# Optimization experiments

Measured on AMD Instinct MI355X. Metric: run time of the kernel, lower is better.

## Reference

```python
import jax, jax.numpy as jnp
import numpy as np

NUM_EXPERTS = 8
HIDDEN = 1024
TOKENS = 8192


def setup_inputs() -> dict:
    key = jax.random.key(0)
    k1, k2, k3, k4 = jax.random.split(key, 4)
    inp = jax.random.normal(k1, (TOKENS, HIDDEN), dtype=jnp.float32)
    gate = jax.random.normal(k2, (TOKENS, NUM_EXPERTS), dtype=jnp.float32)
    # expert parameters: one dense layer per expert (H -> H)
    W = jax.random.normal(k3, (NUM_EXPERTS, HIDDEN, HIDDEN), dtype=jnp.float32) / np.sqrt(HIDDEN)
    b = jax.random.normal(k4, (NUM_EXPERTS, HIDDEN), dtype=jnp.float32) * 0.01
    return {"input": inp, "gate": gate, "W": W, "b": b}


def reference(input, gate, W, b):
    # Routing: softmax over router logits, top-1 expert per token.
    probs = jax.nn.softmax(gate, axis=-1)            # [T, E]
    expert_idx = jnp.argmax(probs, axis=-1)          # [T]
    top_p = jnp.take_along_axis(probs, expert_idx[:, None], axis=-1)[:, 0]  # [T]

    # Dispatch + grouped GEMM (computed densely for all experts, then masked):
    # y[e, t, d] = input[t, :] @ W[e] + b[e]
    y = jnp.einsum("th,ehd->etd", input, W) + b[:, None, :]  # [E, T, H]

    # Combine: select the routed expert's output, scaled by its gate prob.
    dispatch = jax.nn.one_hot(expert_idx, NUM_EXPERTS, dtype=input.dtype) * top_p[:, None]  # [T, E]
    out = jnp.einsum("etd,te->td", y, dispatch)      # [T, H]
    return out
```

## Files before the change

kernel.cpp:

```cpp
#include <hip/hip_runtime.h>
#include <hip/hip_bf16.h>
#include <cstdint>
#include <cstddef>

#define TOK 8192
#define HID 1024
#define NE 8

typedef __bf16 bf16x4 __attribute__((ext_vector_type(4)));
typedef __bf16 bf16x8 __attribute__((ext_vector_type(8)));
typedef float floatx4 __attribute__((ext_vector_type(4)));

static __device__ __forceinline__ __bf16 f2bf(float x) {
    unsigned u = __builtin_bit_cast(unsigned, x);
    u += 0x7fffu + ((u >> 16) & 1u);
    unsigned short hs = (unsigned short)(u >> 16);
    return __builtin_bit_cast(__bf16, hs);
}

__global__ void prep_kernel(const float* __restrict__ X, const float* __restrict__ gate,
                            const float* __restrict__ W,
                            __bf16* __restrict__ Xb, __bf16* __restrict__ Wt,
                            float* __restrict__ scale, int* __restrict__ counts,
                            int* __restrict__ list) {
    const int b = blockIdx.x;
    const int t = threadIdx.x;

    if (b < 4096) {
        size_t idx = (size_t)b * 256 + t;
        const float4 a0 = *(const float4*)(X + idx * 8);
        const float4 a1 = *(const float4*)(X + idx * 8 + 4);
        bf16x8 v;
        v[0] = f2bf(a0.x); v[1] = f2bf(a0.y); v[2] = f2bf(a0.z); v[3] = f2bf(a0.w);
        v[4] = f2bf(a1.x); v[5] = f2bf(a1.y); v[6] = f2bf(a1.z); v[7] = f2bf(a1.w);
        *(bf16x8*)(Xb + idx * 8) = v;

        if (b < 32) {
            __shared__ int hcnt[NE];
            __shared__ int hbase[NE];
            if (t < NE) hcnt[t] = 0;
            __syncthreads();
            int tok = b * 256 + t;
            float g[NE];
#pragma unroll
            for (int j = 0; j < NE; j++) g[j] = gate[tok * NE + j];
            float gm = g[0]; int best = 0;
#pragma unroll
            for (int j = 1; j < NE; j++) {
                if (g[j] > gm) { gm = g[j]; best = j; }
            }
            float s = 0.f;
#pragma unroll
            for (int j = 0; j < NE; j++) s += __expf(g[j] - gm);
            scale[tok] = 1.0f / s;
            int lpos = atomicAdd(&hcnt[best], 1);
            __syncthreads();
            if (t < NE) hbase[t] = atomicAdd(&counts[t], hcnt[t]);
            __syncthreads();
            list[best * TOK + hbase[best] + lpos] = tok;
        }
    } else {
        const int bb = b - 4096;
        const int e = bb >> 8;
        const int tk = (bb >> 4) & 15;
        const int tn = bb & 15;
        const int k0 = tk * 64, n0 = tn * 64;

        __shared__ float ld[64][65];
        {
            const int r4 = t >> 4, c4 = t & 15;
#pragma unroll
            for (int i = 0; i < 4; i++) {
                int kl = r4 + 16 * i;
                float4 v = *(const float4*)(W + ((size_t)e * HID + (k0 + kl)) * HID + n0 + c4 * 4);
                ld[kl][c4 * 4 + 0] = v.x; ld[kl][c4 * 4 + 1] = v.y;
                ld[kl][c4 * 4 + 2] = v.z; ld[kl][c4 * 4 + 3] = v.w;
            }
        }
        __syncthreads();
        {
            const int nl = t >> 2, kc2 = t & 3;
#pragma unroll
            for (int h = 0; h < 2; h++) {
                int c = kc2 + 4 * h;
                bf16x8 v;
#pragma unroll
                for (int j = 0; j < 8; j++) v[j] = f2bf(ld[c * 8 + j][nl]);
                *(bf16x8*)(Wt + ((size_t)e * HID + n0 + nl) * HID + k0 + c * 8) = v;
            }
        }
    }
}

__launch_bounds__(256)
__global__ void moe_gemm_bf16(const __bf16* __restrict__ Xb, const __bf16* __restrict__ Wt,
                              const float* __restrict__ Bias, const float* __restrict__ scale,
                              const int* __restrict__ counts, const int* __restrict__ list,
                              float* __restrict__ out) {
    const int bid = blockIdx.x;
    const int nt = bid & 7;
    const int mt = (bid >> 3) & 63;
    const int e  = bid >> 9;

    const int cnt = counts[e];
    if (mt * 128 >= cnt) return;
    const int mvalid = min(128, cnt - mt * 128);
    const int n0 = nt * 128;

    __shared__ __bf16 As[128 * 64];
    __shared__ __bf16 Bs[128 * 64];
    __shared__ int   tok[128];
    __shared__ float scl[128];

    const int tid  = threadIdx.x;
    const int lane = tid & 63;
    const int wave = tid >> 6;

    if (tid < 128) {
        int g = mt * 128 + tid;
        int tk = (g < cnt) ? list[e * TOK + g] : 0;
        tok[tid] = tk;
        scl[tid] = (g < cnt) ? scale[tk] : 0.f;
    }
    __syncthreads();

    const int srow = lane >> 3;
    const int gchunk = ((lane & 7) ^ srow) * 8;
    const __bf16* aptr[4];
    const __bf16* bptr[4];
#pragma unroll
    for (int i = 0; i < 4; i++) {
        int r = wave * 32 + i * 8 + srow;
        aptr[i] = Xb + (size_t)tok[r] * HID + gchunk;
        bptr[i] = Wt + ((size_t)e * HID + n0 + r) * HID + gchunk;
    }

    const int ln = lane & 15;
    const int q  = lane >> 4;
    const int wm = (wave >> 1) * 64;
    const int wn = (wave & 1) * 64;
    const int rsw = ln & 7;

    floatx4 acc[4][4];
#pragma unroll
    for (int mi = 0; mi < 4; mi++)
#pragma unroll
        for (int ni = 0; ni < 4; ni++) acc[mi][ni] = (floatx4){0.f, 0.f, 0.f, 0.f};

    for (int k0 = 0; k0 < HID; k0 += 64) {
#pragma unroll
        for (int i = 0; i < 4; i++) {
            __builtin_amdgcn_global_load_lds(
                (const __attribute__((address_space(1))) void*)(aptr[i] + k0),
                (__attribute__((address_space(3))) void*)(&As[(wave * 32 + i * 8) * 64]),
                16, 0, 0);
            __builtin_amdgcn_global_load_lds(
                (const __attribute__((address_space(1))) void*)(bptr[i] + k0),
                (__attribute__((address_space(3))) void*)(&Bs[(wave * 32 + i * 8) * 64]),
                16, 0, 0);
        }
        __syncthreads();

#pragma unroll
        for (int kk = 0; kk < 64; kk += 32) {
            const int cb = (kk >> 3) + q;
            const int pos = (cb ^ rsw) * 8;
            bf16x8 af[4], bfv[4];
#pragma unroll
            for (int mi = 0; mi < 4; mi++)
                af[mi] = *(const bf16x8*)(&As[(wm + mi * 16 + ln) * 64 + pos]);
#pragma unroll
            for (int ni = 0; ni < 4; ni++)
                bfv[ni] = *(const bf16x8*)(&Bs[(wn + ni * 16 + ln) * 64 + pos]);
#pragma unroll
            for (int mi = 0; mi < 4; mi++)
#pragma unroll
                for (int ni = 0; ni < 4; ni++)
                    acc[mi][ni] = __builtin_amdgcn_mfma_f32_16x16x32_bf16(
                        af[mi], bfv[ni], acc[mi][ni], 0, 0, 0);
        }
        __syncthreads();
    }

    float bn[4];
#pragma unroll
    for (int ni = 0; ni < 4; ni++) bn[ni] = Bias[e * HID + n0 + wn + ni * 16 + ln];

#pragma unroll
    for (int mi = 0; mi < 4; mi++) {
#pragma unroll
        for (int r = 0; r < 4; r++) {
            int row = wm + mi * 16 + q * 4 + r;
            if (row < mvalid) {
                int t = tok[row];
                float sc = scl[row];
                size_t ob = (size_t)t * HID + n0 + wn + ln;
#pragma unroll
                for (int ni = 0; ni < 4; ni++)
                    out[ob + ni * 16] = sc * (acc[mi][ni][r] + bn[ni]);
            }
        }
    }
}

__launch_bounds__(256)
__global__ void moe_gemm_fb(const float* __restrict__ X, const float* __restrict__ W,
                            const float* __restrict__ Bias, const float* __restrict__ scale,
                            const int* __restrict__ counts, const int* __restrict__ list,
                            float* __restrict__ out) {
    const int bid = blockIdx.x;
    const int e  = bid >> 9;
    const int nt = (bid >> 6) & 7;
    const int mt = bid & 63;
    const int cnt = counts[e];
    if (mt * 128 >= cnt) return;
    const int mvalid = min(128, cnt - mt * 128);
    const int n0 = nt * 128;

    __shared__ __bf16 As[128 * 64];
    __shared__ __bf16 Bs[128 * 64];
    __shared__ int   tok[128];
    __shared__ float scl[128];

    const int tid = threadIdx.x;
    if (tid < 128) {
        int g = mt * 128 + tid;
        int tk = (g < cnt) ? list[e * TOK + g] : 0;
        tok[tid] = tk;
        scl[tid] = (g < cnt) ? scale[tk] : 0.f;
    }
    __syncthreads();

    const int c4 = tid & 15;
    const float* rp[8];
    bool rv[8];
#pragma unroll
    for (int i = 0; i < 8; i++) {
        int m = (tid >> 4) + 16 * i;
        rv[i] = (m < mvalid);
        rp[i] = X + (size_t)tok[m] * HID;
    }
    const int n4 = tid & 31;
    const int kb = tid >> 5;
    const float* wbase = W + (size_t)e * HID * HID + (size_t)(kb * 8) * HID + n0 + n4 * 4;

    const int lane = tid & 63;
    const int ln = lane & 15;
    const int q  = lane >> 4;
    const int wave = tid >> 6;
    const int wm = (wave >> 1) * 64;
    const int wn = (wave & 1) * 64;

    floatx4 acc[4][4];
#pragma unroll
    for (int mi = 0; mi < 4; mi++)
#pragma unroll
        for (int ni = 0; ni < 4; ni++) acc[mi][ni] = (floatx4){0.f, 0.f, 0.f, 0.f};

    for (int k0 = 0; k0 < HID; k0 += 64) {
#pragma unroll
        for (int i = 0; i < 8; i++) {
            int m = (tid >> 4) + 16 * i;
            float4 v = make_float4(0.f, 0.f, 0.f, 0.f);
            if (rv[i]) v = *(const float4*)(rp[i] + k0 + c4 * 4);
            bf16x4 b4;
            b4[0] = f2bf(v.x); b4[1] = f2bf(v.y); b4[2] = f2bf(v.z); b4[3] = f2bf(v.w);
            int chunk = c4 >> 1;
            int addr = m * 64 + ((chunk ^ (m & 7)) * 8) + (c4 & 1) * 4;
            *(bf16x4*)(&As[addr]) = b4;
        }
        {
            const float* wp = wbase + (size_t)k0 * HID;
            float4 rr[8];
#pragma unroll
            for (int r = 0; r < 8; r++) rr[r] = *(const float4*)(wp + (size_t)r * HID);
#pragma unroll
            for (int j = 0; j < 4; j++) {
                int n = n4 * 4 + j;
                int c = kb ^ (n & 7);
                bf16x8 pk;
                pk[0] = f2bf(j == 0 ? rr[0].x : j == 1 ? rr[0].y : j == 2 ? rr[0].z : rr[0].w);
                pk[1] = f2bf(j == 0 ? rr[1].x : j == 1 ? rr[1].y : j == 2 ? rr[1].z : rr[1].w);
                pk[2] = f2bf(j == 0 ? rr[2].x : j == 1 ? rr[2].y : j == 2 ? rr[2].z : rr[2].w);
                pk[3] = f2bf(j == 0 ? rr[3].x : j == 1 ? rr[3].y : j == 2 ? rr[3].z : rr[3].w);
                pk[4] = f2bf(j == 0 ? rr[4].x : j == 1 ? rr[4].y : j == 2 ? rr[4].z : rr[4].w);
                pk[5] = f2bf(j == 0 ? rr[5].x : j == 1 ? rr[5].y : j == 2 ? rr[5].z : rr[5].w);
                pk[6] = f2bf(j == 0 ? rr[6].x : j == 1 ? rr[6].y : j == 2 ? rr[6].z : rr[6].w);
                pk[7] = f2bf(j == 0 ? rr[7].x : j == 1 ? rr[7].y : j == 2 ? rr[7].z : rr[7].w);
                *(bf16x8*)(&Bs[n * 64 + c * 8]) = pk;
            }
        }
        __syncthreads();
#pragma unroll
        for (int kk = 0; kk < 64; kk += 32) {
            const int cbase = (kk >> 3) + q;
            bf16x8 af[4], bfv[4];
#pragma unroll
            for (int mi = 0; mi < 4; mi++) {
                int row = wm + mi * 16 + ln;
                af[mi] = *(const bf16x8*)(&As[row * 64 + ((cbase ^ (row & 7)) * 8)]);
            }
#pragma unroll
            for (int ni = 0; ni < 4; ni++) {
                int n = wn + ni * 16 + ln;
                bfv[ni] = *(const bf16x8*)(&Bs[n * 64 + ((cbase ^ (n & 7)) * 8)]);
            }
#pragma unroll
            for (int mi = 0; mi < 4; mi++)
#pragma unroll
                for (int ni = 0; ni < 4; ni++)
                    acc[mi][ni] = __builtin_amdgcn_mfma_f32_16x16x32_bf16(
                        af[mi], bfv[ni], acc[mi][ni], 0, 0, 0);
        }
        __syncthreads();
    }

    float bn[4];
#pragma unroll
    for (int ni = 0; ni < 4; ni++) bn[ni] = Bias[e * HID + n0 + wn + ni * 16 + ln];
#pragma unroll
    for (int mi = 0; mi < 4; mi++) {
#pragma unroll
        for (int r = 0; r < 4; r++) {
            int row = wm + mi * 16 + q * 4 + r;
            if (row < mvalid) {
                int t = tok[row];
                float sc = scl[row];
                size_t ob = (size_t)t * HID + n0 + wn + ln;
#pragma unroll
                for (int ni = 0; ni < 4; ni++)
                    out[ob + ni * 16] = sc * (acc[mi][ni][r] + bn[ni]);
            }
        }
    }
}

__global__ void zero_counts_kernel(int* counts) {
    if (threadIdx.x < NE) counts[threadIdx.x] = 0;
}

__global__ void route_fb_kernel(const float* __restrict__ gate, float* __restrict__ scale,
                                int* __restrict__ counts, int* __restrict__ list) {
    int t = blockIdx.x * blockDim.x + threadIdx.x;
    if (t >= TOK) return;
    float g[NE];
#pragma unroll
    for (int j = 0; j < NE; j++) g[j] = gate[t * NE + j];
    float gm = g[0]; int best = 0;
#pragma unroll
    for (int j = 1; j < NE; j++) {
        if (g[j] > gm) { gm = g[j]; best = j; }
    }
    float s = 0.f;
#pragma unroll
    for (int j = 0; j < NE; j++) s += __expf(g[j] - gm);
    scale[t] = 1.0f / s;
    int pos = atomicAdd(&counts[best], 1);
    list[best * TOK + pos] = t;
}

extern "C" void kernel_launch(void* const* d_in, const int* in_sizes, int n_in,
                              void* d_out, int out_size, void* d_ws, size_t ws_size,
                              hipStream_t stream) {
    const float* X    = (const float*)d_in[0];
    const float* G    = (const float*)d_in[1];
    const float* W    = (const float*)d_in[2];
    const float* Bias = (const float*)d_in[3];
    float* out = (float*)d_out;

    float* scale = (float*)d_ws;
    int* counts  = (int*)((char*)d_ws + 32768);
    int* list    = (int*)((char*)d_ws + 36864);
    __bf16* Xb   = (__bf16*)((char*)d_ws + 299008);
    __bf16* Wt   = (__bf16*)((char*)d_ws + 299008 + 16777216);
    const size_t need = 299008 + 2 * 16777216ULL;

    hipMemsetAsync(counts, 0, NE * sizeof(int), stream);

    if (ws_size >= need) {
        prep_kernel<<<6144, 256, 0, stream>>>(X, G, W, Xb, Wt, scale, counts, list);
        moe_gemm_bf16<<<NE * 64 * 8, 256, 0, stream>>>(Xb, Wt, Bias, scale, counts, list, out);
    } else {
        route_fb_kernel<<<TOK / 256, 256, 0, stream>>>(G, scale, counts, list);
        moe_gemm_fb<<<NE * 64 * 8, 256, 0, stream>>>(X, W, Bias, scale, counts, list, out);
    }
}
```

Before: 150.4 us.

## Double-buffer GEMM LDS tiles, register-transpose W prep, interleave expert blocks

The bf16 GEMM now double-buffers its A/B tiles in LDS. The next k-tile is issued via global_load_lds before computing the current one, and one barrier per iteration is removed. The W transpose/convert in prep_kernel now does an 8x8 register transpose per thread over 256-wide k tiles instead of going through an LDS staging buffer, which cuts the prep grid from 6144 to 4608 blocks. Block-to-(expert, n, m) mapping puts expert in the low bits so early-exit blocks are spread out, and outputs use nontemporal stores. LDS usage doubles, which may reduce occupancy.

```diff
diff --git a/kernel.cpp b/kernel.cpp
--- a/kernel.cpp
+++ b/kernel.cpp
@@ -61,33 +61,29 @@
         }
     } else {
         const int bb = b - 4096;
-        const int e = bb >> 8;
-        const int tk = (bb >> 4) & 15;
-        const int tn = bb & 15;
-        const int k0 = tk * 64, n0 = tn * 64;
-
-        __shared__ float ld[64][65];
-        {
-            const int r4 = t >> 4, c4 = t & 15;
-#pragma unroll
-            for (int i = 0; i < 4; i++) {
-                int kl = r4 + 16 * i;
-                float4 v = *(const float4*)(W + ((size_t)e * HID + (k0 + kl)) * HID + n0 + c4 * 4);
-                ld[kl][c4 * 4 + 0] = v.x; ld[kl][c4 * 4 + 1] = v.y;
-                ld[kl][c4 * 4 + 2] = v.z; ld[kl][c4 * 4 + 3] = v.w;
-            }
-        }
-        __syncthreads();
-        {
-            const int nl = t >> 2, kc2 = t & 3;
-#pragma unroll
-            for (int h = 0; h < 2; h++) {
-                int c = kc2 + 4 * h;
-                bf16x8 v;
-#pragma unroll
-                for (int j = 0; j < 8; j++) v[j] = f2bf(ld[c * 8 + j][nl]);
-                *(bf16x8*)(Wt + ((size_t)e * HID + n0 + nl) * HID + k0 + c * 8) = v;
-            }
+        const int e  = bb >> 6;
+        const int kt = (bb >> 4) & 3;
+        const int nt = bb & 15;
+        const int k0 = kt * 256, n0 = nt * 64;
+        const int ka = t >> 3;
+        const int nb = t & 7;
+
+        const float* src = W + ((size_t)e * HID + k0 + ka * 8) * HID + n0 + nb * 8;
+        float rr[8][8];
+#pragma unroll
+        for (int i = 0; i < 8; i++) {
+            float4 x = *(const float4*)(src + (size_t)i * HID);
+            float4 y = *(const float4*)(src + (size_t)i * HID + 4);
+            rr[i][0] = x.x; rr[i][1] = x.y; rr[i][2] = x.z; rr[i][3] = x.w;
+            rr[i][4] = y.x; rr[i][5] = y.y; rr[i][6] = y.z; rr[i][7] = y.w;
+        }
+        __bf16* dst = Wt + ((size_t)e * HID + n0 + nb * 8) * HID + k0 + ka * 8;
+#pragma unroll
+        for (int j = 0; j < 8; j++) {
+            bf16x8 v;
+#pragma unroll
+            for (int i = 0; i < 8; i++) v[i] = f2bf(rr[i][j]);
+            *(bf16x8*)(dst + (size_t)j * HID) = v;
         }
     }
 }
@@ -98,17 +94,17 @@
                               const int* __restrict__ counts, const int* __restrict__ list,
                               float* __restrict__ out) {
     const int bid = blockIdx.x;
-    const int nt = bid & 7;
-    const int mt = (bid >> 3) & 63;
-    const int e  = bid >> 9;
+    const int e  = bid & 7;
+    const int nt = (bid >> 3) & 7;
+    const int mt = bid >> 6;
 
     const int cnt = counts[e];
     if (mt * 128 >= cnt) return;
     const int mvalid = min(128, cnt - mt * 128);
     const int n0 = nt * 128;
 
-    __shared__ __bf16 As[128 * 64];
-    __shared__ __bf16 Bs[128 * 64];
+    __shared__ __bf16 As[2][128 * 64];
+    __shared__ __bf16 Bs[2][128 * 64];
     __shared__ int   tok[128];
     __shared__ float scl[128];
 
@@ -147,19 +143,26 @@
 #pragma unroll
         for (int ni = 0; ni < 4; ni++) acc[mi][ni] = (floatx4){0.f, 0.f, 0.f, 0.f};
 
-    for (int k0 = 0; k0 < HID; k0 += 64) {
+    auto stage = [&](int kt, int buf) {
+        const int k0 = kt * 64;
 #pragma unroll
         for (int i = 0; i < 4; i++) {
             __builtin_amdgcn_global_load_lds(
                 (const __attribute__((address_space(1))) void*)(aptr[i] + k0),
-                (__attribute__((address_space(3))) void*)(&As[(wave * 32 + i * 8) * 64]),
+                (__attribute__((address_space(3))) void*)(&As[buf][(wave * 32 + i * 8) * 64]),
                 16, 0, 0);
             __builtin_amdgcn_global_load_lds(
                 (const __attribute__((address_space(1))) void*)(bptr[i] + k0),
-                (__attribute__((address_space(3))) void*)(&Bs[(wave * 32 + i * 8) * 64]),
+                (__attribute__((address_space(3))) void*)(&Bs[buf][(wave * 32 + i * 8) * 64]),
                 16, 0, 0);
         }
+    };
+
+    stage(0, 0);
+    for (int kt = 0; kt < 16; ++kt) {
         __syncthreads();
+        if (kt < 15) stage(kt + 1, (kt + 1) & 1);
+        const int buf = kt & 1;
 
 #pragma unroll
         for (int kk = 0; kk < 64; kk += 32) {
@@ -168,10 +171,10 @@
             bf16x8 af[4], bfv[4];
 #pragma unroll
             for (int mi = 0; mi < 4; mi++)
-                af[mi] = *(const bf16x8*)(&As[(wm + mi * 16 + ln) * 64 + pos]);
+                af[mi] = *(const bf16x8*)(&As[buf][(wm + mi * 16 + ln) * 64 + pos]);
 #pragma unroll
             for (int ni = 0; ni < 4; ni++)
-                bfv[ni] = *(const bf16x8*)(&Bs[(wn + ni * 16 + ln) * 64 + pos]);
+                bfv[ni] = *(const bf16x8*)(&Bs[buf][(wn + ni * 16 + ln) * 64 + pos]);
 #pragma unroll
             for (int mi = 0; mi < 4; mi++)
 #pragma unroll
@@ -179,7 +182,6 @@
                     acc[mi][ni] = __builtin_amdgcn_mfma_f32_16x16x32_bf16(
                         af[mi], bfv[ni], acc[mi][ni], 0, 0, 0);
         }
-        __syncthreads();
     }
 
     float bn[4];
@@ -197,7 +199,8 @@
                 size_t ob = (size_t)t * HID + n0 + wn + ln;
 #pragma unroll
                 for (int ni = 0; ni < 4; ni++)
-                    out[ob + ni * 16] = sc * (acc[mi][ni][r] + bn[ni]);
+                    __builtin_nontemporal_store(sc * (acc[mi][ni][r] + bn[ni]),
+                                                &out[ob + ni * 16]);
             }
         }
     }
@@ -335,10 +338,6 @@
     }
 }
 
-__global__ void zero_counts_kernel(int* counts) {
-    if (threadIdx.x < NE) counts[threadIdx.x] = 0;
-}
-
 __global__ void route_fb_kernel(const float* __restrict__ gate, float* __restrict__ scale,
                                 int* __restrict__ counts, int* __restrict__ list) {
     int t = blockIdx.x * blockDim.x + threadIdx.x;
@@ -378,7 +377,7 @@
     hipMemsetAsync(counts, 0, NE * sizeof(int), stream);
 
     if (ws_size >= need) {
-        prep_kernel<<<6144, 256, 0, stream>>>(X, G, W, Xb, Wt, scale, counts, list);
+        prep_kernel<<<4608, 256, 0, stream>>>(X, G, W, Xb, Wt, scale, counts, list);
         moe_gemm_bf16<<<NE * 64 * 8, 256, 0, stream>>>(Xb, Wt, Bias, scale, counts, list, out);
     } else {
         route_fb_kernel<<<TOK / 256, 256, 0, stream>>>(G, scale, counts, list);
```

After: 160.2 us. 6.5% more time.
